# Kernel tuning notes

Measured on AMD Instinct MI355X. Metric: run time of the kernel, lower is better.

The kernel has to match this reference:

```python
import jax, jax.numpy as jnp
import numpy as np

# WGS84 constants
_A = 6378137.0
_E2 = 6.69437999014e-3  # first eccentricity squared

ALPHA = 1.0
GAMMA = 2.0
DYNAMIC_GAMMA = True
SCALE_FACTOR = 1.0


def _geodetic_to_ecef(lat_rad, lon_rad, h):
    sl, cl = jnp.sin(lat_rad), jnp.cos(lat_rad)
    so, co = jnp.sin(lon_rad), jnp.cos(lon_rad)
    N = _A / jnp.sqrt(1.0 - _E2 * sl * sl)
    x = (N + h) * cl * co
    y = (N + h) * cl * so
    z = (N * (1.0 - _E2) + h) * sl
    return jnp.stack([x, y, z], axis=-1)


def setup_inputs() -> dict:
    key = jax.random.key(0)
    k1, k2, k3, k4 = jax.random.split(key, 4)
    B = 4_000_000
    lat = jax.random.uniform(k1, (B,), jnp.float32, -80.0, 80.0)    # degrees
    lon = jax.random.uniform(k2, (B,), jnp.float32, -180.0, 180.0)  # degrees
    h = jax.random.uniform(k3, (B,), jnp.float32, 0.0, 1000.0)      # meters
    targets = jnp.stack([lat, lon, h], axis=1)
    ref_ecef = _geodetic_to_ecef(jnp.deg2rad(lat), jnp.deg2rad(lon), h)
    # predicted ECEF = true ECEF + ~meters of noise -> realistic GNSS error
    inputs = ref_ecef + 2.0 * jax.random.normal(k4, (B, 3), jnp.float32)
    return {"inputs": inputs, "targets": targets}


def _ecef_to_enu(pred_ecef, gt_geodetic):
    # Batched version of the per-sample ecef_to_enu_torch loop.
    lat = jnp.deg2rad(gt_geodetic[:, 0])
    lon = jnp.deg2rad(gt_geodetic[:, 1])
    h = gt_geodetic[:, 2]
    ref = _geodetic_to_ecef(lat, lon, h)
    d = pred_ecef - ref  # [B,3]
    sl, cl = jnp.sin(lat), jnp.cos(lat)
    so, co = jnp.sin(lon), jnp.cos(lon)
    dx, dy, dz = d[:, 0], d[:, 1], d[:, 2]
    e = -so * dx + co * dy
    n = -sl * co * dx - sl * so * dy + cl * dz
    u = cl * co * dx + cl * so * dy + sl * dz
    return jnp.stack([e, n, u], axis=1)  # [B,3]


def reference(inputs, targets):
    enu_errors = _ecef_to_enu(inputs, targets)                 # [B,3]
    squared_dist = jnp.sqrt(jnp.sum(enu_errors * enu_errors, axis=1))  # L2 norm [B]
    base_loss = squared_dist
    if DYNAMIC_GAMMA:
        dyn_gamma = GAMMA * jnp.exp(-SCALE_FACTOR * base_loss)
    else:
        dyn_gamma = GAMMA
    focal_weight = jnp.power(1.0 - jnp.sqrt(squared_dist / (jnp.max(squared_dist) + 1e-8)), dyn_gamma)
    focal_loss = ALPHA * focal_weight * base_loss
    return jnp.sqrt(jnp.mean(focal_loss * focal_loss))
```

## Files before the change

### kernel.cpp

```cpp
#include <hip/hip_runtime.h>
#include <math.h>


#define THREADS 256
#define PART_OFF 64
#define PART_CAP 8192
#define DIST_OFF (64 + PART_CAP * 8)

__device__ __forceinline__ void sincos_small(double x, double& s_out, double& c_out) {
    const double TWO_OVER_PI = 0.636619772367581343076;
    const double PIO2_HI = 1.57079632679489655800e+00;
    const double PIO2_LO = 6.12323399573676603587e-17;
    double kd = rint(x * TWO_OVER_PI);
    int q = ((int)kd) & 3;
    double r = fma(-kd, PIO2_HI, x);
    r = fma(-kd, PIO2_LO, r);
    double r2 = r * r;

    double ps = 1.58969099521155010221e-10;
    ps = fma(ps, r2, -2.50507602534068634195e-08);
    ps = fma(ps, r2, 2.75573137070700676789e-06);
    ps = fma(ps, r2, -1.98412698298579493134e-04);
    ps = fma(ps, r2, 8.33333333332248946124e-03);
    ps = fma(ps, r2, -1.66666666666666324348e-01);
    double s = fma(r2 * r, ps, r);

    double pc = -1.13596475577881948265e-11;
    pc = fma(pc, r2, 2.08757232129817482790e-09);
    pc = fma(pc, r2, -2.75573143513906633035e-07);
    pc = fma(pc, r2, 2.48015872894767294178e-05);
    pc = fma(pc, r2, -1.38888888888741095749e-03);
    pc = fma(pc, r2, 4.16666666666666019037e-02);
    double c = fma(r2 * r2, pc, fma(-0.5, r2, 1.0));

    double sr = (q & 1) ? c : s;
    double cr = (q & 1) ? s : c;
    sr = (q & 2) ? -sr : sr;
    cr = ((q + 1) & 2) ? -cr : cr;
    s_out = sr;
    c_out = cr;
}

__device__ __forceinline__ float dist_one(float latd, float lond, float hf,
                                          float px, float py, float pz) {
    const float D2R = (float)0.017453292519943295;
    float latr = latd * D2R;
    float lonr = lond * D2R;

    double sl, cl, so, co;
    sincos_small((double)latr, sl, cl);
    sincos_small((double)lonr, so, co);
    double h = (double)hf;

    const double A  = 6378137.0;
    const double E2 = 0.00669437999014;
    double w = fma(-E2 * sl, sl, 1.0);
    double y = fma(-0.5, w, 1.5);
    y = y * fma(-0.5 * w, y * y, 1.5);
    y = y * fma(-0.5 * w, y * y, 1.5);
    double N  = A * y;
    double Nh = N + h;
    double x  = Nh * cl * co;
    double yy = Nh * cl * so;
    double z  = fma(N, -E2, N + h) * sl;

    double dx = (double)px - x;
    double dy = (double)py - yy;
    double dz = (double)pz - z;

    double e = -so * dx + co * dy;
    double n = -sl * co * dx - sl * so * dy + cl * dz;
    double u =  cl * co * dx + cl * so * dy + sl * dz;

    return sqrtf((float)(e * e + n * n + u * u));
}

__global__ void k_pass1(const float* __restrict__ inp,
                        const float* __restrict__ tgt,
                        float* __restrict__ dist_arr,
                        float* __restrict__ blockmax,
                        long B) {
    long ngroups = (B + 3) >> 2;
    long gstride = (long)gridDim.x * blockDim.x;
    float lmax = 0.0f;
    for (long g = (long)blockIdx.x * blockDim.x + threadIdx.x; g < ngroups; g += gstride) {
        long base = g << 2;
        if (base + 3 < B) {
            const float4* t4 = (const float4*)(tgt + 3 * base);
            float4 ta = t4[0], tb = t4[1], tc = t4[2];
            const float4* p4 = (const float4*)(inp + 3 * base);
            float4 pa = p4[0], pb = p4[1], pc = p4[2];
            float d0 = dist_one(ta.x, ta.y, ta.z, pa.x, pa.y, pa.z);
            float d1 = dist_one(ta.w, tb.x, tb.y, pa.w, pb.x, pb.y);
            float d2 = dist_one(tb.z, tb.w, tc.x, pb.z, pb.w, pc.x);
            float d3 = dist_one(tc.y, tc.z, tc.w, pc.y, pc.z, pc.w);
            if (dist_arr) *(float4*)(dist_arr + base) = make_float4(d0, d1, d2, d3);
            lmax = fmaxf(lmax, fmaxf(fmaxf(d0, d1), fmaxf(d2, d3)));
        } else {
            for (long i = base; i < B; ++i) {
                float d = dist_one(tgt[3*i], tgt[3*i+1], tgt[3*i+2],
                                   inp[3*i], inp[3*i+1], inp[3*i+2]);
                if (dist_arr) dist_arr[i] = d;
                lmax = fmaxf(lmax, d);
            }
        }
    }
    for (int off = 32; off > 0; off >>= 1)
        lmax = fmaxf(lmax, __shfl_down(lmax, off, 64));
    __shared__ float smax[THREADS / 64];
    if ((threadIdx.x & 63) == 0) smax[threadIdx.x >> 6] = lmax;
    __syncthreads();
    if (threadIdx.x == 0) {
        float m = smax[0];
        for (int w = 1; w < THREADS / 64; ++w) m = fmaxf(m, smax[w]);
        blockmax[blockIdx.x] = m;
    }
}

__global__ void k_max(const float* __restrict__ blockmax, int n,
                      float* __restrict__ maxslot) {
    float m = 0.0f;
    for (int i = threadIdx.x; i < n; i += blockDim.x) m = fmaxf(m, blockmax[i]);
    for (int off = 32; off > 0; off >>= 1)
        m = fmaxf(m, __shfl_down(m, off, 64));
    __shared__ float smax[THREADS / 64];
    if ((threadIdx.x & 63) == 0) smax[threadIdx.x >> 6] = m;
    __syncthreads();
    if (threadIdx.x == 0) {
        float mm = smax[0];
        for (int w = 1; w < THREADS / 64; ++w) mm = fmaxf(mm, smax[w]);
        *maxslot = mm;
    }
}

__device__ __forceinline__ double focal2(float d, float denom) {
    float g = 2.0f * __expf(-d);
    float b = 1.0f - sqrtf(d / denom);
    b = fmaxf(b, 0.0f);
    float wgt = __builtin_amdgcn_exp2f(g * __log2f(b));
    float fl = wgt * d;
    return (double)fl * (double)fl;
}

__global__ void k_pass2(const float* __restrict__ dist_arr,
                        const float* __restrict__ inp,
                        const float* __restrict__ tgt,
                        const float* __restrict__ maxslot,
                        double* __restrict__ partials,
                        long B) {
    float denom = *maxslot + 1e-8f;
    long ngroups = (B + 3) >> 2;
    long gstride = (long)gridDim.x * blockDim.x;
    double acc = 0.0;
    for (long g = (long)blockIdx.x * blockDim.x + threadIdx.x; g < ngroups; g += gstride) {
        long base = g << 2;
        if (base + 3 < B) {
            float d0, d1, d2, d3;
            if (dist_arr) {
                float4 d4 = *(const float4*)(dist_arr + base);
                d0 = d4.x; d1 = d4.y; d2 = d4.z; d3 = d4.w;
            } else {
                const float4* t4 = (const float4*)(tgt + 3 * base);
                float4 ta = t4[0], tb = t4[1], tc = t4[2];
                const float4* p4 = (const float4*)(inp + 3 * base);
                float4 pa = p4[0], pb = p4[1], pc = p4[2];
                d0 = dist_one(ta.x, ta.y, ta.z, pa.x, pa.y, pa.z);
                d1 = dist_one(ta.w, tb.x, tb.y, pa.w, pb.x, pb.y);
                d2 = dist_one(tb.z, tb.w, tc.x, pb.z, pb.w, pc.x);
                d3 = dist_one(tc.y, tc.z, tc.w, pc.y, pc.z, pc.w);
            }
            acc += focal2(d0, denom) + focal2(d1, denom)
                 + focal2(d2, denom) + focal2(d3, denom);
        } else {
            for (long i = base; i < B; ++i) {
                float d = dist_arr ? dist_arr[i]
                                   : dist_one(tgt[3*i], tgt[3*i+1], tgt[3*i+2],
                                              inp[3*i], inp[3*i+1], inp[3*i+2]);
                acc += focal2(d, denom);
            }
        }
    }
    for (int off = 32; off > 0; off >>= 1)
        acc += __shfl_down(acc, off, 64);
    __shared__ double lds[THREADS / 64];
    if ((threadIdx.x & 63) == 0) lds[threadIdx.x >> 6] = acc;
    __syncthreads();
    if (threadIdx.x == 0) {
        double s = lds[0];
        for (int w = 1; w < THREADS / 64; ++w) s += lds[w];
        partials[blockIdx.x] = s;
    }
}

__global__ void k_final(const double* __restrict__ partials, int nparts,
                        float* __restrict__ out, long B) {
    double acc = 0.0;
    for (int i = threadIdx.x; i < nparts; i += blockDim.x) acc += partials[i];
    for (int off = 32; off > 0; off >>= 1)
        acc += __shfl_down(acc, off, 64);
    __shared__ double lds[THREADS / 64];
    if ((threadIdx.x & 63) == 0) lds[threadIdx.x >> 6] = acc;
    __syncthreads();
    if (threadIdx.x == 0) {
        double s = lds[0];
        for (int w = 1; w < THREADS / 64; ++w) s += lds[w];
        out[0] = (float)sqrt(s / (double)B);
    }
}

extern "C" void kernel_launch(void* const* d_in, const int* in_sizes, int n_in,
                              void* d_out, int out_size, void* d_ws, size_t ws_size,
                              hipStream_t stream) {
    const float* inp = (const float*)d_in[0];
    const float* tgt = (const float*)d_in[1];
    float* out = (float*)d_out;
    long B = (long)in_sizes[0] / 3;

    float* maxslot = (float*)d_ws;
    float* blockmax = (float*)((char*)d_ws + PART_OFF);
    double* partials = (double*)((char*)d_ws + PART_OFF);
    float* dist_arr = nullptr;
    size_t need = (size_t)DIST_OFF + (size_t)B * sizeof(float);
    if (ws_size >= need) dist_arr = (float*)((char*)d_ws + DIST_OFF);

    long ngroups = (B + 3) >> 2;
    int nblocks = (int)((ngroups + THREADS - 1) / THREADS);
    if (nblocks > PART_CAP) nblocks = PART_CAP;
    if (nblocks < 1) nblocks = 1;

    k_pass1<<<nblocks, THREADS, 0, stream>>>(inp, tgt, dist_arr, blockmax, B);
    k_max<<<1, THREADS, 0, stream>>>(blockmax, nblocks, maxslot);
    k_pass2<<<nblocks, THREADS, 0, stream>>>(dist_arr, inp, tgt, maxslot, partials, B);
    k_final<<<1, THREADS, 0, stream>>>(partials, nblocks, out, B);
}
```

Before: 134.2 us.

## Fuse all passes into one cooperative kernel with LDS-resident distances

Replaces the four-kernel pipeline with a single cooperative launch of 512 blocks. Each block keeps its slice of per-point distances in shared memory (32 KB) across grid-wide syncs, so the global distance array round-trip and three extra kernel launches go away. The grid max and final sum are done after grid.sync barriers. The cost is lower occupancy from the large LDS footprint and launch bound, a fixed 512-block grid, and the overhead of grid syncs. Larger inputs fall back to the old path.

```diff
diff --git a/kernel.cpp b/kernel.cpp
--- a/kernel.cpp
+++ b/kernel.cpp
@@ -1,11 +1,17 @@
 #include <hip/hip_runtime.h>
+#include <hip/hip_cooperative_groups.h>
 #include <math.h>
 
+namespace cg = cooperative_groups;
+
 
 #define THREADS 256
+#define GRID 512
+#define GPB_MAX 2048
 #define PART_OFF 64
+#define PART2_OFF (64 + GRID * 4)
 #define PART_CAP 8192
-#define DIST_OFF (64 + PART_CAP * 8)
+#define DIST_OFF (65600)
 
 __device__ __forceinline__ void sincos_small(double x, double& s_out, double& c_out) {
     const double TWO_OVER_PI = 0.636619772367581343076;
@@ -75,11 +81,126 @@
     return sqrtf((float)(e * e + n * n + u * u));
 }
 
-__global__ void k_pass1(const float* __restrict__ inp,
-                        const float* __restrict__ tgt,
-                        float* __restrict__ dist_arr,
-                        float* __restrict__ blockmax,
-                        long B) {
+__device__ __forceinline__ double focal2(float d, float denom) {
+    float g = 2.0f * __expf(-d);
+    float b = 1.0f - sqrtf(d / denom);
+    b = fmaxf(b, 0.0f);
+    float wgt = __builtin_amdgcn_exp2f(g * __log2f(b));
+    float fl = wgt * d;
+    return (double)fl * (double)fl;
+}
+
+__global__ __launch_bounds__(THREADS, 2)
+void k_fused(const float* __restrict__ inp,
+             const float* __restrict__ tgt,
+             float* __restrict__ blockmax,
+             double* __restrict__ partials,
+             float* __restrict__ out,
+             long B) {
+    cg::grid_group grid = cg::this_grid();
+    __shared__ float dist_lds[GPB_MAX * 4];
+    __shared__ float smax[THREADS / 64];
+    __shared__ double sacc[THREADS / 64];
+    __shared__ float sbcast;
+
+    long ngroups = (B + 3) >> 2;
+    long gpb = (ngroups + gridDim.x - 1) / gridDim.x;
+    long g0 = (long)blockIdx.x * gpb;
+    long g1 = g0 + gpb; if (g1 > ngroups) g1 = ngroups;
+    int tid = threadIdx.x;
+
+    float lmax = 0.0f;
+    for (long g = g0 + tid; g < g1; g += THREADS) {
+        long base = g << 2;
+        int li = (int)(g - g0) << 2;
+        if (base + 3 < B) {
+            const float4* t4 = (const float4*)(tgt + 3 * base);
+            float4 ta = t4[0], tb = t4[1], tc = t4[2];
+            const float4* p4 = (const float4*)(inp + 3 * base);
+            float4 pa = p4[0], pb = p4[1], pc = p4[2];
+            float d0 = dist_one(ta.x, ta.y, ta.z, pa.x, pa.y, pa.z);
+            float d1 = dist_one(ta.w, tb.x, tb.y, pa.w, pb.x, pb.y);
+            float d2 = dist_one(tb.z, tb.w, tc.x, pb.z, pb.w, pc.x);
+            float d3 = dist_one(tc.y, tc.z, tc.w, pc.y, pc.z, pc.w);
+            *(float4*)(dist_lds + li) = make_float4(d0, d1, d2, d3);
+            lmax = fmaxf(lmax, fmaxf(fmaxf(d0, d1), fmaxf(d2, d3)));
+        } else {
+            for (long i = base; i < B; ++i) {
+                float d = dist_one(tgt[3*i], tgt[3*i+1], tgt[3*i+2],
+                                   inp[3*i], inp[3*i+1], inp[3*i+2]);
+                dist_lds[li + (int)(i - base)] = d;
+                lmax = fmaxf(lmax, d);
+            }
+        }
+    }
+    for (int off = 32; off > 0; off >>= 1)
+        lmax = fmaxf(lmax, __shfl_down(lmax, off, 64));
+    if ((tid & 63) == 0) smax[tid >> 6] = lmax;
+    __syncthreads();
+    if (tid == 0) {
+        float m = smax[0];
+        for (int w = 1; w < THREADS / 64; ++w) m = fmaxf(m, smax[w]);
+        blockmax[blockIdx.x] = m;
+    }
+
+    grid.sync();
+
+    float m = 0.0f;
+    for (int i = tid; i < (int)gridDim.x; i += THREADS) m = fmaxf(m, blockmax[i]);
+    for (int off = 32; off > 0; off >>= 1)
+        m = fmaxf(m, __shfl_down(m, off, 64));
+    if ((tid & 63) == 0) smax[tid >> 6] = m;
+    __syncthreads();
+    if (tid == 0) {
+        float mm = smax[0];
+        for (int w = 1; w < THREADS / 64; ++w) mm = fmaxf(mm, smax[w]);
+        sbcast = mm;
+    }
+    __syncthreads();
+    float denom = sbcast + 1e-8f;
+
+    double acc = 0.0;
+    for (long g = g0 + tid; g < g1; g += THREADS) {
+        long base = g << 2;
+        int li = (int)(g - g0) << 2;
+        if (base + 3 < B) {
+            float4 d4 = *(const float4*)(dist_lds + li);
+            acc += focal2(d4.x, denom) + focal2(d4.y, denom)
+                 + focal2(d4.z, denom) + focal2(d4.w, denom);
+        } else {
+            for (long i = base; i < B; ++i)
+                acc += focal2(dist_lds[li + (int)(i - base)], denom);
+        }
+    }
+    for (int off = 32; off > 0; off >>= 1)
+        acc += __shfl_down(acc, off, 64);
+    if ((tid & 63) == 0) sacc[tid >> 6] = acc;
+    __syncthreads();
+    if (tid == 0) {
+        double s = sacc[0];
+        for (int w = 1; w < THREADS / 64; ++w) s += sacc[w];
+        partials[blockIdx.x] = s;
+    }
+
+    grid.sync();
+
+    if (blockIdx.x == 0) {
+        double a = 0.0;
+        for (int i = tid; i < (int)gridDim.x; i += THREADS) a += partials[i];
+        for (int off = 32; off > 0; off >>= 1)
+            a += __shfl_down(a, off, 64);
+        if ((tid & 63) == 0) sacc[tid >> 6] = a;
+        __syncthreads();
+        if (tid == 0) {
+            double s = sacc[0];
+            for (int w = 1; w < THREADS / 64; ++w) s += sacc[w];
+            out[0] = (float)sqrt(s / (double)B);
+        }
+    }
+}
+
+__global__ void k_pass1(const float* __restrict__ inp, const float* __restrict__ tgt,
+                        float* __restrict__ dist_arr, float* __restrict__ blockmax, long B) {
     long ngroups = (B + 3) >> 2;
     long gstride = (long)gridDim.x * blockDim.x;
     float lmax = 0.0f;
@@ -117,8 +238,7 @@
     }
 }
 
-__global__ void k_max(const float* __restrict__ blockmax, int n,
-                      float* __restrict__ maxslot) {
+__global__ void k_max(const float* __restrict__ blockmax, int n, float* __restrict__ maxslot) {
     float m = 0.0f;
     for (int i = threadIdx.x; i < n; i += blockDim.x) m = fmaxf(m, blockmax[i]);
     for (int off = 32; off > 0; off >>= 1)
@@ -133,21 +253,9 @@
     }
 }
 
-__device__ __forceinline__ double focal2(float d, float denom) {
-    float g = 2.0f * __expf(-d);
-    float b = 1.0f - sqrtf(d / denom);
-    b = fmaxf(b, 0.0f);
-    float wgt = __builtin_amdgcn_exp2f(g * __log2f(b));
-    float fl = wgt * d;
-    return (double)fl * (double)fl;
-}
-
-__global__ void k_pass2(const float* __restrict__ dist_arr,
-                        const float* __restrict__ inp,
-                        const float* __restrict__ tgt,
-                        const float* __restrict__ maxslot,
-                        double* __restrict__ partials,
-                        long B) {
+__global__ void k_pass2(const float* __restrict__ dist_arr, const float* __restrict__ inp,
+                        const float* __restrict__ tgt, const float* __restrict__ maxslot,
+                        double* __restrict__ partials, long B) {
     float denom = *maxslot + 1e-8f;
     long ngroups = (B + 3) >> 2;
     long gstride = (long)gridDim.x * blockDim.x;
@@ -216,20 +324,28 @@
     float* out = (float*)d_out;
     long B = (long)in_sizes[0] / 3;
 
-    float* maxslot = (float*)d_ws;
     float* blockmax = (float*)((char*)d_ws + PART_OFF);
-    double* partials = (double*)((char*)d_ws + PART_OFF);
-    float* dist_arr = nullptr;
-    size_t need = (size_t)DIST_OFF + (size_t)B * sizeof(float);
-    if (ws_size >= need) dist_arr = (float*)((char*)d_ws + DIST_OFF);
-
-    long ngroups = (B + 3) >> 2;
-    int nblocks = (int)((ngroups + THREADS - 1) / THREADS);
-    if (nblocks > PART_CAP) nblocks = PART_CAP;
-    if (nblocks < 1) nblocks = 1;
-
-    k_pass1<<<nblocks, THREADS, 0, stream>>>(inp, tgt, dist_arr, blockmax, B);
-    k_max<<<1, THREADS, 0, stream>>>(blockmax, nblocks, maxslot);
-    k_pass2<<<nblocks, THREADS, 0, stream>>>(dist_arr, inp, tgt, maxslot, partials, B);
-    k_final<<<1, THREADS, 0, stream>>>(partials, nblocks, out, B);
-}
+    double* partials = (double*)((char*)d_ws + PART2_OFF);
+
+    long coop_cap = (long)GRID * GPB_MAX * 4;
+    if (B <= coop_cap) {
+        void* args[] = { (void*)&inp, (void*)&tgt, (void*)&blockmax,
+                         (void*)&partials, (void*)&out, (void*)&B };
+        hipLaunchCooperativeKernel((const void*)k_fused, dim3(GRID), dim3(THREADS),
+                                   args, 0, stream);
+    } else {
+        float* maxslot = (float*)d_ws;
+        double* partials2 = (double*)((char*)d_ws + PART2_OFF);
+        float* dist_arr = nullptr;
+        size_t need = (size_t)DIST_OFF + (size_t)B * sizeof(float);
+        if (ws_size >= need) dist_arr = (float*)((char*)d_ws + DIST_OFF);
+        long ngroups = (B + 3) >> 2;
+        int nblocks = (int)((ngroups + THREADS - 1) / THREADS);
+        if (nblocks > PART_CAP) nblocks = PART_CAP;
+        if (nblocks < 1) nblocks = 1;
+        k_pass1<<<nblocks, THREADS, 0, stream>>>(inp, tgt, dist_arr, blockmax, B);
+        k_max<<<1, THREADS, 0, stream>>>(blockmax, nblocks, maxslot);
+        k_pass2<<<nblocks, THREADS, 0, stream>>>(dist_arr, inp, tgt, maxslot, partials2, B);
+        k_final<<<1, THREADS, 0, stream>>>(partials2, nblocks, out, B);
+    }
+}
```

Measured after the change: 240.8 us. +79.5%, slower.

## Interleave sincos for eight angles and fold max reduction into pass2

Applied to the files above, without the earlier changes.

The sincos polynomial evaluation is restructured to process eight angles at once in lockstep, exposing independent FP64 FMA chains for more instruction-level parallelism. The separate k_max launch is removed; every pass2 block now re-reduces the block maxima itself before its main loop. Launch bounds are added to pass1 to steer register allocation, and the workspace layout is split so blockmax and partials no longer alias. This raises register pressure and repeats a small reduction in every block, in exchange for one fewer launch and better FP64 pipeline utilisation.

```diff
diff --git a/kernel.cpp b/kernel.cpp
--- a/kernel.cpp
+++ b/kernel.cpp
@@ -3,83 +3,112 @@
 
 
 #define THREADS 256
-#define PART_OFF 64
 #define PART_CAP 8192
-#define DIST_OFF (64 + PART_CAP * 8)
-
-__device__ __forceinline__ void sincos_small(double x, double& s_out, double& c_out) {
+#define BMAX_OFF 64
+#define PART_OFF (64 + PART_CAP * 4)
+#define DIST_OFF (1 << 20)
+
+__device__ __forceinline__ void sincos8(const double* __restrict__ x,
+                                        double* __restrict__ s,
+                                        double* __restrict__ c) {
     const double TWO_OVER_PI = 0.636619772367581343076;
     const double PIO2_HI = 1.57079632679489655800e+00;
     const double PIO2_LO = 6.12323399573676603587e-17;
-    double kd = rint(x * TWO_OVER_PI);
-    int q = ((int)kd) & 3;
-    double r = fma(-kd, PIO2_HI, x);
-    r = fma(-kd, PIO2_LO, r);
-    double r2 = r * r;
-
-    double ps = 1.58969099521155010221e-10;
-    ps = fma(ps, r2, -2.50507602534068634195e-08);
-    ps = fma(ps, r2, 2.75573137070700676789e-06);
-    ps = fma(ps, r2, -1.98412698298579493134e-04);
-    ps = fma(ps, r2, 8.33333333332248946124e-03);
-    ps = fma(ps, r2, -1.66666666666666324348e-01);
-    double s = fma(r2 * r, ps, r);
-
-    double pc = -1.13596475577881948265e-11;
-    pc = fma(pc, r2, 2.08757232129817482790e-09);
-    pc = fma(pc, r2, -2.75573143513906633035e-07);
-    pc = fma(pc, r2, 2.48015872894767294178e-05);
-    pc = fma(pc, r2, -1.38888888888741095749e-03);
-    pc = fma(pc, r2, 4.16666666666666019037e-02);
-    double c = fma(r2 * r2, pc, fma(-0.5, r2, 1.0));
-
-    double sr = (q & 1) ? c : s;
-    double cr = (q & 1) ? s : c;
-    sr = (q & 2) ? -sr : sr;
-    cr = ((q + 1) & 2) ? -cr : cr;
-    s_out = sr;
-    c_out = cr;
+
+    double kd[8], r[8], r2[8];
+    int q[8];
+#pragma unroll
+    for (int j = 0; j < 8; ++j) {
+        kd[j] = rint(x[j] * TWO_OVER_PI);
+        q[j] = ((int)kd[j]) & 3;
+    }
+#pragma unroll
+    for (int j = 0; j < 8; ++j) {
+        double rr = fma(-kd[j], PIO2_HI, x[j]);
+        r[j] = fma(-kd[j], PIO2_LO, rr);
+        r2[j] = r[j] * r[j];
+    }
+    double ps[8], pc[8];
+#pragma unroll
+    for (int j = 0; j < 8; ++j) { ps[j] = 1.58969099521155010221e-10;
+                                  pc[j] = -1.13596475577881948265e-11; }
+#pragma unroll
+    for (int j = 0; j < 8; ++j) { ps[j] = fma(ps[j], r2[j], -2.50507602534068634195e-08);
+                                  pc[j] = fma(pc[j], r2[j],  2.08757232129817482790e-09); }
+#pragma unroll
+    for (int j = 0; j < 8; ++j) { ps[j] = fma(ps[j], r2[j],  2.75573137070700676789e-06);
+                                  pc[j] = fma(pc[j], r2[j], -2.75573143513906633035e-07); }
+#pragma unroll
+    for (int j = 0; j < 8; ++j) { ps[j] = fma(ps[j], r2[j], -1.98412698298579493134e-04);
+                                  pc[j] = fma(pc[j], r2[j],  2.48015872894767294178e-05); }
+#pragma unroll
+    for (int j = 0; j < 8; ++j) { ps[j] = fma(ps[j], r2[j],  8.33333333332248946124e-03);
+                                  pc[j] = fma(pc[j], r2[j], -1.38888888888741095749e-03); }
+#pragma unroll
+    for (int j = 0; j < 8; ++j) { ps[j] = fma(ps[j], r2[j], -1.66666666666666324348e-01);
+                                  pc[j] = fma(pc[j], r2[j],  4.16666666666666019037e-02); }
+#pragma unroll
+    for (int j = 0; j < 8; ++j) {
+        double sv = fma(r2[j] * r[j], ps[j], r[j]);
+        double cv = fma(r2[j] * r2[j], pc[j], fma(-0.5, r2[j], 1.0));
+        double sr = (q[j] & 1) ? cv : sv;
+        double cr = (q[j] & 1) ? sv : cv;
+        s[j] = (q[j] & 2) ? -sr : sr;
+        c[j] = ((q[j] + 1) & 2) ? -cr : cr;
+    }
+}
+
+__device__ __forceinline__ void dist_group4(const float* __restrict__ lat,
+                                            const float* __restrict__ lon,
+                                            const float* __restrict__ hh,
+                                            const float* __restrict__ px,
+                                            const float* __restrict__ py,
+                                            const float* __restrict__ pz,
+                                            float* __restrict__ dout) {
+    const float D2R = (float)0.017453292519943295;
+    double x[8], s8[8], c8[8];
+#pragma unroll
+    for (int j = 0; j < 4; ++j) x[j] = (double)(lat[j] * D2R);
+#pragma unroll
+    for (int j = 0; j < 4; ++j) x[4 + j] = (double)(lon[j] * D2R);
+    sincos8(x, s8, c8);
+
+    const double A = 6378137.0, E2 = 0.00669437999014;
+#pragma unroll
+    for (int j = 0; j < 4; ++j) {
+        double sl = s8[j], cl = c8[j], so = s8[4 + j], co = c8[4 + j];
+        double h = (double)hh[j];
+        double w = fma(-E2 * sl, sl, 1.0);
+        double y = fma(-0.5, w, 1.5);
+        y = y * fma(-0.5 * w, y * y, 1.5);
+        y = y * fma(-0.5 * w, y * y, 1.5);
+        double N = A * y, Nh = N + h;
+        double X = Nh * cl * co;
+        double Y = Nh * cl * so;
+        double Z = fma(N, -E2, N + h) * sl;
+        double dx = (double)px[j] - X;
+        double dy = (double)py[j] - Y;
+        double dz = (double)pz[j] - Z;
+        double e = -so * dx + co * dy;
+        double n = -sl * co * dx - sl * so * dy + cl * dz;
+        double u =  cl * co * dx + cl * so * dy + sl * dz;
+        dout[j] = sqrtf((float)(e * e + n * n + u * u));
+    }
 }
 
 __device__ __forceinline__ float dist_one(float latd, float lond, float hf,
-                                          float px, float py, float pz) {
-    const float D2R = (float)0.017453292519943295;
-    float latr = latd * D2R;
-    float lonr = lond * D2R;
-
-    double sl, cl, so, co;
-    sincos_small((double)latr, sl, cl);
-    sincos_small((double)lonr, so, co);
-    double h = (double)hf;
-
-    const double A  = 6378137.0;
-    const double E2 = 0.00669437999014;
-    double w = fma(-E2 * sl, sl, 1.0);
-    double y = fma(-0.5, w, 1.5);
-    y = y * fma(-0.5 * w, y * y, 1.5);
-    y = y * fma(-0.5 * w, y * y, 1.5);
-    double N  = A * y;
-    double Nh = N + h;
-    double x  = Nh * cl * co;
-    double yy = Nh * cl * so;
-    double z  = fma(N, -E2, N + h) * sl;
-
-    double dx = (double)px - x;
-    double dy = (double)py - yy;
-    double dz = (double)pz - z;
-
-    double e = -so * dx + co * dy;
-    double n = -sl * co * dx - sl * so * dy + cl * dz;
-    double u =  cl * co * dx + cl * so * dy + sl * dz;
-
-    return sqrtf((float)(e * e + n * n + u * u));
-}
-
-__global__ void k_pass1(const float* __restrict__ inp,
-                        const float* __restrict__ tgt,
-                        float* __restrict__ dist_arr,
-                        float* __restrict__ blockmax,
-                        long B) {
+                                          float pxx, float pyy, float pzz) {
+    float lat[4] = {latd, latd, latd, latd}, lon[4] = {lond, lond, lond, lond};
+    float hh[4] = {hf, hf, hf, hf};
+    float px[4] = {pxx, pxx, pxx, pxx}, py[4] = {pyy, pyy, pyy, pyy}, pz[4] = {pzz, pzz, pzz, pzz};
+    float d[4];
+    dist_group4(lat, lon, hh, px, py, pz, d);
+    return d[0];
+}
+
+__global__ __launch_bounds__(THREADS, 3)
+void k_pass1(const float* __restrict__ inp, const float* __restrict__ tgt,
+             float* __restrict__ dist_arr, float* __restrict__ blockmax, long B) {
     long ngroups = (B + 3) >> 2;
     long gstride = (long)gridDim.x * blockDim.x;
     float lmax = 0.0f;
@@ -90,12 +119,16 @@
             float4 ta = t4[0], tb = t4[1], tc = t4[2];
             const float4* p4 = (const float4*)(inp + 3 * base);
             float4 pa = p4[0], pb = p4[1], pc = p4[2];
-            float d0 = dist_one(ta.x, ta.y, ta.z, pa.x, pa.y, pa.z);
-            float d1 = dist_one(ta.w, tb.x, tb.y, pa.w, pb.x, pb.y);
-            float d2 = dist_one(tb.z, tb.w, tc.x, pb.z, pb.w, pc.x);
-            float d3 = dist_one(tc.y, tc.z, tc.w, pc.y, pc.z, pc.w);
-            if (dist_arr) *(float4*)(dist_arr + base) = make_float4(d0, d1, d2, d3);
-            lmax = fmaxf(lmax, fmaxf(fmaxf(d0, d1), fmaxf(d2, d3)));
+            float lat[4] = {ta.x, ta.w, tb.z, tc.y};
+            float lon[4] = {ta.y, tb.x, tb.w, tc.z};
+            float hh[4]  = {ta.z, tb.y, tc.x, tc.w};
+            float px[4]  = {pa.x, pa.w, pb.z, pc.y};
+            float py[4]  = {pa.y, pb.x, pb.w, pc.z};
+            float pz[4]  = {pa.z, pb.y, pc.x, pc.w};
+            float d[4];
+            dist_group4(lat, lon, hh, px, py, pz, d);
+            if (dist_arr) *(float4*)(dist_arr + base) = make_float4(d[0], d[1], d[2], d[3]);
+            lmax = fmaxf(lmax, fmaxf(fmaxf(d[0], d[1]), fmaxf(d[2], d[3])));
         } else {
             for (long i = base; i < B; ++i) {
                 float d = dist_one(tgt[3*i], tgt[3*i+1], tgt[3*i+2],
@@ -117,22 +150,6 @@
     }
 }
 
-__global__ void k_max(const float* __restrict__ blockmax, int n,
-                      float* __restrict__ maxslot) {
-    float m = 0.0f;
-    for (int i = threadIdx.x; i < n; i += blockDim.x) m = fmaxf(m, blockmax[i]);
-    for (int off = 32; off > 0; off >>= 1)
-        m = fmaxf(m, __shfl_down(m, off, 64));
-    __shared__ float smax[THREADS / 64];
-    if ((threadIdx.x & 63) == 0) smax[threadIdx.x >> 6] = m;
-    __syncthreads();
-    if (threadIdx.x == 0) {
-        float mm = smax[0];
-        for (int w = 1; w < THREADS / 64; ++w) mm = fmaxf(mm, smax[w]);
-        *maxslot = mm;
-    }
-}
-
 __device__ __forceinline__ double focal2(float d, float denom) {
     float g = 2.0f * __expf(-d);
     float b = 1.0f - sqrtf(d / denom);
@@ -145,14 +162,31 @@
 __global__ void k_pass2(const float* __restrict__ dist_arr,
                         const float* __restrict__ inp,
                         const float* __restrict__ tgt,
-                        const float* __restrict__ maxslot,
-                        double* __restrict__ partials,
-                        long B) {
-    float denom = *maxslot + 1e-8f;
+                        const float* __restrict__ blockmax, int nb1,
+                        double* __restrict__ partials, long B) {
+    __shared__ float smax[THREADS / 64];
+    __shared__ double sacc[THREADS / 64];
+    __shared__ float sb;
+    int tid = threadIdx.x;
+
+    float m = 0.0f;
+    for (int i = tid; i < nb1; i += THREADS) m = fmaxf(m, blockmax[i]);
+    for (int off = 32; off > 0; off >>= 1)
+        m = fmaxf(m, __shfl_down(m, off, 64));
+    if ((tid & 63) == 0) smax[tid >> 6] = m;
+    __syncthreads();
+    if (tid == 0) {
+        float mm = smax[0];
+        for (int w = 1; w < THREADS / 64; ++w) mm = fmaxf(mm, smax[w]);
+        sb = mm;
+    }
+    __syncthreads();
+    float denom = sb + 1e-8f;
+
     long ngroups = (B + 3) >> 2;
     long gstride = (long)gridDim.x * blockDim.x;
     double acc = 0.0;
-    for (long g = (long)blockIdx.x * blockDim.x + threadIdx.x; g < ngroups; g += gstride) {
+    for (long g = (long)blockIdx.x * blockDim.x + tid; g < ngroups; g += gstride) {
         long base = g << 2;
         if (base + 3 < B) {
             float d0, d1, d2, d3;
@@ -164,10 +198,15 @@
                 float4 ta = t4[0], tb = t4[1], tc = t4[2];
                 const float4* p4 = (const float4*)(inp + 3 * base);
                 float4 pa = p4[0], pb = p4[1], pc = p4[2];
-                d0 = dist_one(ta.x, ta.y, ta.z, pa.x, pa.y, pa.z);
-                d1 = dist_one(ta.w, tb.x, tb.y, pa.w, pb.x, pb.y);
-                d2 = dist_one(tb.z, tb.w, tc.x, pb.z, pb.w, pc.x);
-                d3 = dist_one(tc.y, tc.z, tc.w, pc.y, pc.z, pc.w);
+                float lat[4] = {ta.x, ta.w, tb.z, tc.y};
+                float lon[4] = {ta.y, tb.x, tb.w, tc.z};
+                float hh[4]  = {ta.z, tb.y, tc.x, tc.w};
+                float px[4]  = {pa.x, pa.w, pb.z, pc.y};
+                float py[4]  = {pa.y, pb.x, pb.w, pc.z};
+                float pz[4]  = {pa.z, pb.y, pc.x, pc.w};
+                float d[4];
+                dist_group4(lat, lon, hh, px, py, pz, d);
+                d0 = d[0]; d1 = d[1]; d2 = d[2]; d3 = d[3];
             }
             acc += focal2(d0, denom) + focal2(d1, denom)
                  + focal2(d2, denom) + focal2(d3, denom);
@@ -182,12 +221,11 @@
     }
     for (int off = 32; off > 0; off >>= 1)
         acc += __shfl_down(acc, off, 64);
-    __shared__ double lds[THREADS / 64];
-    if ((threadIdx.x & 63) == 0) lds[threadIdx.x >> 6] = acc;
-    __syncthreads();
-    if (threadIdx.x == 0) {
-        double s = lds[0];
-        for (int w = 1; w < THREADS / 64; ++w) s += lds[w];
+    if ((tid & 63) == 0) sacc[tid >> 6] = acc;
+    __syncthreads();
+    if (tid == 0) {
+        double s = sacc[0];
+        for (int w = 1; w < THREADS / 64; ++w) s += sacc[w];
         partials[blockIdx.x] = s;
     }
 }
@@ -216,8 +254,7 @@
     float* out = (float*)d_out;
     long B = (long)in_sizes[0] / 3;
 
-    float* maxslot = (float*)d_ws;
-    float* blockmax = (float*)((char*)d_ws + PART_OFF);
+    float* blockmax = (float*)((char*)d_ws + BMAX_OFF);
     double* partials = (double*)((char*)d_ws + PART_OFF);
     float* dist_arr = nullptr;
     size_t need = (size_t)DIST_OFF + (size_t)B * sizeof(float);
@@ -229,7 +266,6 @@
     if (nblocks < 1) nblocks = 1;
 
     k_pass1<<<nblocks, THREADS, 0, stream>>>(inp, tgt, dist_arr, blockmax, B);
-    k_max<<<1, THREADS, 0, stream>>>(blockmax, nblocks, maxslot);
-    k_pass2<<<nblocks, THREADS, 0, stream>>>(dist_arr, inp, tgt, maxslot, partials, B);
+    k_pass2<<<nblocks, THREADS, 0, stream>>>(dist_arr, inp, tgt, blockmax, nblocks, partials, B);
     k_final<<<1, THREADS, 0, stream>>>(partials, nblocks, out, B);
 }
```

New measurement: 136.9 us. 1.02x slower.
